# Optimization experiments

Hardware: AMD Instinct MI355X
Metric: run time of the kernel (lower is better)

## Reference

```python
import jax, jax.numpy as jnp
import numpy as np

N = 50000
E = 800000
D_IN = 128
D_OUT = 128


def setup_inputs() -> dict:
    key = jax.random.key(0)
    ks = jax.random.split(key, 12)
    x = jax.random.normal(ks[0], (N, D_IN), dtype=jnp.float32)
    W1 = jax.random.normal(ks[1], (D_IN, D_OUT), dtype=jnp.float32) * (1.0 / np.sqrt(D_IN))
    b1 = jnp.zeros((D_OUT,), dtype=jnp.float32)
    W2 = jax.random.normal(ks[2], (D_IN, D_OUT), dtype=jnp.float32) * (1.0 / np.sqrt(D_IN))
    b2 = jnp.zeros((D_OUT,), dtype=jnp.float32)
    # inverted-dropout masks, p=0.5 -> values in {0, 2}
    def mask(k):
        return jnp.where(jax.random.uniform(k, (N, D_IN)) < 0.5, 0.0, 2.0).astype(jnp.float32)
    mask_pos1 = mask(ks[3])
    mask_neg1 = mask(ks[4])
    mask_pos2 = mask(ks[5])
    mask_neg2 = mask(ks[6])
    edge_index1 = jax.random.randint(ks[7], (2, E), 0, N, dtype=jnp.int32)
    edge_index2 = jax.random.randint(ks[8], (2, E), 0, N, dtype=jnp.int32)
    perm1 = jax.random.permutation(ks[9], N).astype(jnp.int32)
    perm2 = jax.random.permutation(ks[10], N).astype(jnp.int32)
    return dict(x=x, W1=W1, b1=b1, W2=W2, b2=b2,
                mask_pos1=mask_pos1, mask_neg1=mask_neg1,
                mask_pos2=mask_pos2, mask_neg2=mask_neg2,
                edge_index1=edge_index1, edge_index2=edge_index2,
                perm1=perm1, perm2=perm2)


def gcn_conv(x, W, b, edge_index):
    """PyG GCNConv: add self-loops, symmetric normalization, then x@W aggregation + bias."""
    n = x.shape[0]
    xw = x @ W  # [N, D_OUT]
    loops = jnp.arange(n, dtype=edge_index.dtype)
    src = jnp.concatenate([edge_index[0], loops])
    dst = jnp.concatenate([edge_index[1], loops])
    deg = jax.ops.segment_sum(jnp.ones_like(dst, dtype=xw.dtype), dst, num_segments=n)
    dinv = jax.lax.rsqrt(jnp.maximum(deg, 1.0))  # deg >= 1 due to self-loops
    norm = dinv[src] * dinv[dst]                 # [E+N]
    msg = xw[src] * norm[:, None]                # [E+N, D_OUT]
    out = jax.ops.segment_sum(msg, dst, num_segments=n)
    return out + b


def _branch(x, W, b, edge_index, mask_pos, mask_neg, perm):
    pos_h = jax.nn.relu(gcn_conv(x * mask_pos, W, b, edge_index))
    neg_in = (x * mask_neg)[perm]
    neg_h = jax.nn.relu(gcn_conv(neg_in, W, b, edge_index))
    summary = jnp.mean(pos_h, axis=0, keepdims=True)  # [1, D_OUT]
    return pos_h, neg_h, summary


def reference(x, W1, b1, W2, b2, mask_pos1, mask_neg1, mask_pos2, mask_neg2,
              edge_index1, edge_index2, perm1, perm2):
    p1, n1, s1 = _branch(x, W1, b1, edge_index1, mask_pos1, mask_neg1, perm1)
    p2, n2, s2 = _branch(x, W2, b2, edge_index2, mask_pos2, mask_neg2, perm2)
    return (p1, n1, s1, p2, n2, s2)
```

## Files before the change

kernel.cpp:

```cpp
#include <hip/hip_runtime.h>
#include <hip/hip_fp16.h>

#define NN 50000
#define NE 800000
#define D 128
#define BKT_BLOCKS 1024
#define GEMM_BLOCKS 3128
#define NBKT 64
#define BW 782
#define SCAP 2048

typedef _Float16 half8_t __attribute__((ext_vector_type(8)));
typedef _Float16 half4_t __attribute__((ext_vector_type(4)));
typedef float f32x4 __attribute__((ext_vector_type(4)));

__global__ void k_init(float* s1, float* s2, int* bcnt,
                       const float* __restrict__ W1, const float* __restrict__ W2,
                       _Float16* wt1, _Float16* wt2,
                       const int* __restrict__ perm1, const int* __restrict__ perm2,
                       int* pinv1, int* pinv2) {
    int i = blockIdx.x * 256 + threadIdx.x;
    if (i < NN) { pinv1[perm1[i]] = i; pinv2[perm2[i]] = i; }
    if (i < 1024) bcnt[i] = 0;
    if (i < D) { s1[i] = 0.f; s2[i] = 0.f; }
    if (i < 16384) {
        int n = i >> 7, k = i & 127;
        wt1[n * 128 + k] = (_Float16)W1[k * 128 + n];
        wt2[n * 128 + k] = (_Float16)W2[k * 128 + n];
    }
}

__launch_bounds__(256)
__global__ void k_bucket_gemm(const int* __restrict__ src1, const int* __restrict__ dst1,
                              const int* __restrict__ src2, const int* __restrict__ dst2,
                              int* bcnt, int2* bsd1, int2* bsd2,
                              const _Float16* __restrict__ wt1, const _Float16* __restrict__ wt2,
                              const float* __restrict__ x,
                              const float* __restrict__ mp1, const float* __restrict__ mn1,
                              const float* __restrict__ mp2, const float* __restrict__ mn2,
                              const int* __restrict__ pinv1, const int* __restrict__ pinv2,
                              _Float16* xwi1, _Float16* xwi2) {
    __shared__ int lcnt[128], lpos[128], gbase[128];
    __shared__ __align__(16) _Float16 ST[4][16][136];
    int t = threadIdx.x;
    int bid = blockIdx.x;

    if (bid < BKT_BLOCKS) {
        int sl = bid & 7;
        if (t < 128) { lcnt[t] = 0; lpos[t] = 0; }
        __syncthreads();

        int e0 = bid * 256 + t;
        int s1v0=0,d1v0=0,s2v0=0,d2v0=0, s1v1=0,d1v1=0,s2v1=0,d2v1=0;
        int s1v2=0,d1v2=0,s2v2=0,d2v2=0, s1v3=0,d1v3=0,s2v3=0,d2v3=0;
        bool v0 = (e0 + 0 * 262144) < NE;
        bool v1 = (e0 + 1 * 262144) < NE;
        bool v2 = (e0 + 2 * 262144) < NE;
        bool v3 = (e0 + 3 * 262144) < NE;
        if (v0) { int e = e0;             s1v0 = src1[e]; d1v0 = dst1[e]; s2v0 = src2[e]; d2v0 = dst2[e]; }
        if (v1) { int e = e0 + 262144;    s1v1 = src1[e]; d1v1 = dst1[e]; s2v1 = src2[e]; d2v1 = dst2[e]; }
        if (v2) { int e = e0 + 2*262144;  s1v2 = src1[e]; d1v2 = dst1[e]; s2v2 = src2[e]; d2v2 = dst2[e]; }
        if (v3) { int e = e0 + 3*262144;  s1v3 = src1[e]; d1v3 = dst1[e]; s2v3 = src2[e]; d2v3 = dst2[e]; }

        if (v0) { atomicAdd(&lcnt[d1v0 / BW], 1); atomicAdd(&lcnt[NBKT + d2v0 / BW], 1); }
        if (v1) { atomicAdd(&lcnt[d1v1 / BW], 1); atomicAdd(&lcnt[NBKT + d2v1 / BW], 1); }
        if (v2) { atomicAdd(&lcnt[d1v2 / BW], 1); atomicAdd(&lcnt[NBKT + d2v2 / BW], 1); }
        if (v3) { atomicAdd(&lcnt[d1v3 / BW], 1); atomicAdd(&lcnt[NBKT + d2v3 / BW], 1); }
        __syncthreads();
        if (t < 128) gbase[t] = atomicAdd(&bcnt[t * 8 + sl], lcnt[t]);
        __syncthreads();

        #define PLACE(sv, dv) { \
            int r = (dv) / BW; \
            int p = gbase[r] + atomicAdd(&lpos[r], 1); \
            if (p < SCAP) bsd1[(r * 8 + sl) * SCAP + p] = make_int2((sv), (dv)); }
        #define PLACE2(sv, dv) { \
            int r = (dv) / BW; \
            int p = gbase[NBKT + r] + atomicAdd(&lpos[NBKT + r], 1); \
            if (p < SCAP) bsd2[(r * 8 + sl) * SCAP + p] = make_int2((sv), (dv)); }
        if (v0) { PLACE(s1v0, d1v0); PLACE2(s2v0, d2v0); }
        if (v1) { PLACE(s1v1, d1v1); PLACE2(s2v1, d2v1); }
        if (v2) { PLACE(s1v2, d1v2); PLACE2(s2v2, d2v2); }
        if (v3) { PLACE(s1v3, d1v3); PLACE2(s2v3, d2v3); }
        #undef PLACE
        #undef PLACE2
        return;
    }

    int g = bid - BKT_BLOCKS;
    int which = g / 782;
    int bx = g - which * 782;
    const _Float16* wt = (which < 2) ? wt1 : wt2;
    const float* mask = (which == 0) ? mp1 : (which == 1) ? mn1 : (which == 2) ? mp2 : mn2;
    const int* pinv = (which == 1) ? pinv1 : (which == 3) ? pinv2 : nullptr;
    _Float16* out = ((which < 2) ? xwi1 : xwi2) + ((which & 1) ? 128 : 0);

    int wave = t >> 6;
    int lane = t & 63;
    int quad = lane >> 4;
    int m = lane & 15;
    int tile = bx * 4 + wave;
    if (tile * 16 >= NN) return;

    int row = tile * 16 + m;
    const float* xrow = x + (long)row * D;
    const float* mrow = mask + (long)row * D;

    half8_t a[4];
    #pragma unroll
    for (int kk = 0; kk < 4; kk++) {
        int k0 = kk * 32 + quad * 8;
        f32x4 xa = *(const f32x4*)(xrow + k0);
        f32x4 xb = *(const f32x4*)(xrow + k0 + 4);
        f32x4 ma = __builtin_nontemporal_load((const f32x4*)(mrow + k0));
        f32x4 mb = __builtin_nontemporal_load((const f32x4*)(mrow + k0 + 4));
        a[kk][0] = (_Float16)(xa[0] * ma[0]);
        a[kk][1] = (_Float16)(xa[1] * ma[1]);
        a[kk][2] = (_Float16)(xa[2] * ma[2]);
        a[kk][3] = (_Float16)(xa[3] * ma[3]);
        a[kk][4] = (_Float16)(xb[0] * mb[0]);
        a[kk][5] = (_Float16)(xb[1] * mb[1]);
        a[kk][6] = (_Float16)(xb[2] * mb[2]);
        a[kk][7] = (_Float16)(xb[3] * mb[3]);
    }

    f32x4 accs[8];
    #pragma unroll
    for (int nt = 0; nt < 8; nt++) {
        const _Float16* wrow = wt + (nt * 16 + m) * 128 + quad * 8;
        f32x4 acc = {0.f, 0.f, 0.f, 0.f};
        #pragma unroll
        for (int kk = 0; kk < 4; kk++) {
            half8_t w = *(const half8_t*)(wrow + kk * 32);
            acc = __builtin_amdgcn_mfma_f32_16x16x32_f16(w, a[kk], acc, 0, 0, 0);
        }
        accs[nt] = acc;
    }

    int orow = pinv ? pinv[row] : row;
    _Float16* st = &ST[wave][0][0];

    #pragma unroll
    for (int nt = 0; nt < 8; nt++) {
        half4_t h;
        h[0] = (_Float16)accs[nt][0];
        h[1] = (_Float16)accs[nt][1];
        h[2] = (_Float16)accs[nt][2];
        h[3] = (_Float16)accs[nt][3];
        *(half4_t*)(st + m * 136 + nt * 16 + quad * 4) = h;
    }
    #pragma unroll
    for (int p = 0; p < 4; p++) {
        int cc = (lane >> 4) + p * 4;
        half8_t v = *(const half8_t*)(st + m * 136 + cc * 8);
        *(half8_t*)(out + (long)orow * 256 + cc * 8) = v;
    }
}

__launch_bounds__(512)
__global__ void k_build(const int* __restrict__ bcnt,
                        const int2* __restrict__ bsd1, const int2* __restrict__ bsd2,
                        int* rp1, int* rp2, int* col1, int* col2,
                        float* dinv1, float* dinv2) {
    __shared__ int h[1024];
    __shared__ int tsum[512];
    __shared__ int tb[64];
    __shared__ int ns[8];
    __shared__ int bbase;
    int t = threadIdx.x;
    int g = blockIdx.x >> 6;
    int f = blockIdx.x & 63;
    const int2* bsd = (g ? bsd2 : bsd1) + f * 8 * SCAP;
    int* rp = g ? rp2 : rp1;
    int* col = g ? col2 : col1;
    float* dinv = g ? dinv2 : dinv1;

    h[t] = 0; h[t + 512] = 0;
    if (t < 8) {
        int v = bcnt[(g * NBKT + f) * 8 + t];
        ns[t] = (v > SCAP) ? SCAP : v;
    }
    if (t < NBKT) {
        int tot = 0;
        #pragma unroll
        for (int s = 0; s < 8; s++) tot += bcnt[(g * NBKT + t) * 8 + s];
        tb[t] = tot;
    }
    __syncthreads();

    #pragma unroll
    for (int s = 0; s < 8; s++) {
        int n = ns[s];
        const int2* seg = bsd + s * SCAP;
        for (int i = t; i < n; i += 512) atomicAdd(&h[seg[i].y - f * BW], 1);
    }
    __syncthreads();
    if (t == 0) { int b = 0; for (int j = 0; j < f; j++) b += tb[j]; bbase = b; }

    int a0 = h[2 * t], a1 = h[2 * t + 1];
    int s = a0 + a1;
    tsum[t] = s;
    __syncthreads();
    for (int off = 1; off < 512; off <<= 1) {
        int add = (t >= off) ? tsum[t - off] : 0;
        __syncthreads();
        tsum[t] += add;
        __syncthreads();
    }
    int excl = tsum[t] - s + bbase;
    int idx = 2 * t, gd = f * BW + idx;
    int e0 = excl, e1 = excl + a0;
    h[2 * t] = e0; h[2 * t + 1] = e1;
    if (idx < BW && gd < NN)         { rp[gd]     = e0; dinv[gd]     = rsqrtf((float)(a0 + 1)); }
    if (idx + 1 < BW && gd + 1 < NN) { rp[gd + 1] = e1; dinv[gd + 1] = rsqrtf((float)(a1 + 1)); }
    if (f == 63 && t == 0) rp[NN] = NE;
    __syncthreads();

    #pragma unroll
    for (int sg = 0; sg < 8; sg++) {
        int n = ns[sg];
        const int2* seg = bsd + sg * SCAP;
        for (int i = t; i < n; i += 512) {
            int2 e = seg[i];
            int p = atomicAdd(&h[e.y - f * BW], 1);
            col[p] = e.x;
        }
    }
}

__launch_bounds__(256)
__global__ void k_agg(const _Float16* __restrict__ xwi1, const _Float16* __restrict__ xwi2,
                      const int* __restrict__ rp1, const int* __restrict__ col1,
                      const float* __restrict__ dinv1,
                      const int* __restrict__ rp2, const int* __restrict__ col2,
                      const float* __restrict__ dinv2,
                      const float* __restrict__ b1, const float* __restrict__ b2,
                      float* out) {
    int g = blockIdx.y;
    const _Float16* xwi = g ? xwi2 : xwi1;
    const int* rp = g ? rp2 : rp1;
    const int* col = g ? col2 : col1;
    const float* dinv = g ? dinv2 : dinv1;
    const float* bias = g ? b2 : b1;
    float* pos_out = out + (g ? 12800128L : 0L);
    float* neg_out = out + (g ? 19200128L : 6400000L);

    int t = threadIdx.x;
    int wave = t >> 6, lane = t & 63;
    int i = blockIdx.x * 4 + wave;
    if (i >= NN) return;
    int j4 = lane * 4;

    float di = dinv[i];
    half4_t sv = *(const half4_t*)(xwi + (long)i * 256 + j4);
    float a0 = di * (float)sv[0], a1 = di * (float)sv[1];
    float a2 = di * (float)sv[2], a3 = di * (float)sv[3];
    int e0 = rp[i], e1 = rp[i + 1];
    int e = e0;
    for (; e + 8 <= e1; e += 8) {
        int s0 = col[e + 0], s1 = col[e + 1], s2 = col[e + 2], s3 = col[e + 3];
        int s4 = col[e + 4], s5 = col[e + 5], s6 = col[e + 6], s7 = col[e + 7];
        float ds0 = dinv[s0], ds1 = dinv[s1], ds2 = dinv[s2], ds3 = dinv[s3];
        float ds4 = dinv[s4], ds5 = dinv[s5], ds6 = dinv[s6], ds7 = dinv[s7];
        half4_t v0 = *(const half4_t*)(xwi + (long)s0 * 256 + j4);
        half4_t v1 = *(const half4_t*)(xwi + (long)s1 * 256 + j4);
        half4_t v2 = *(const half4_t*)(xwi + (long)s2 * 256 + j4);
        half4_t v3 = *(const half4_t*)(xwi + (long)s3 * 256 + j4);
        half4_t v4 = *(const half4_t*)(xwi + (long)s4 * 256 + j4);
        half4_t v5 = *(const half4_t*)(xwi + (long)s5 * 256 + j4);
        half4_t v6 = *(const half4_t*)(xwi + (long)s6 * 256 + j4);
        half4_t v7 = *(const half4_t*)(xwi + (long)s7 * 256 + j4);
        a0 += ds0*(float)v0[0] + ds1*(float)v1[0] + ds2*(float)v2[0] + ds3*(float)v3[0]
            + ds4*(float)v4[0] + ds5*(float)v5[0] + ds6*(float)v6[0] + ds7*(float)v7[0];
        a1 += ds0*(float)v0[1] + ds1*(float)v1[1] + ds2*(float)v2[1] + ds3*(float)v3[1]
            + ds4*(float)v4[1] + ds5*(float)v5[1] + ds6*(float)v6[1] + ds7*(float)v7[1];
        a2 += ds0*(float)v0[2] + ds1*(float)v1[2] + ds2*(float)v2[2] + ds3*(float)v3[2]
            + ds4*(float)v4[2] + ds5*(float)v5[2] + ds6*(float)v6[2] + ds7*(float)v7[2];
        a3 += ds0*(float)v0[3] + ds1*(float)v1[3] + ds2*(float)v2[3] + ds3*(float)v3[3]
            + ds4*(float)v4[3] + ds5*(float)v5[3] + ds6*(float)v6[3] + ds7*(float)v7[3];
    }
    for (; e + 4 <= e1; e += 4) {
        int s0 = col[e + 0], s1 = col[e + 1], s2 = col[e + 2], s3 = col[e + 3];
        float ds0 = dinv[s0], ds1 = dinv[s1], ds2 = dinv[s2], ds3 = dinv[s3];
        half4_t v0 = *(const half4_t*)(xwi + (long)s0 * 256 + j4);
        half4_t v1 = *(const half4_t*)(xwi + (long)s1 * 256 + j4);
        half4_t v2 = *(const half4_t*)(xwi + (long)s2 * 256 + j4);
        half4_t v3 = *(const half4_t*)(xwi + (long)s3 * 256 + j4);
        a0 += ds0*(float)v0[0] + ds1*(float)v1[0] + ds2*(float)v2[0] + ds3*(float)v3[0];
        a1 += ds0*(float)v0[1] + ds1*(float)v1[1] + ds2*(float)v2[1] + ds3*(float)v3[1];
        a2 += ds0*(float)v0[2] + ds1*(float)v1[2] + ds2*(float)v2[2] + ds3*(float)v3[2];
        a3 += ds0*(float)v0[3] + ds1*(float)v1[3] + ds2*(float)v2[3] + ds3*(float)v3[3];
    }
    for (; e < e1; e++) {
        int s = col[e];
        float ds = dinv[s];
        half4_t v = *(const half4_t*)(xwi + (long)s * 256 + j4);
        a0 += ds*(float)v[0]; a1 += ds*(float)v[1]; a2 += ds*(float)v[2]; a3 += ds*(float)v[3];
    }
    int jj = (lane < 32) ? j4 : (j4 - 128);
    const f32x4* bp = (const f32x4*)(bias + jj);
    f32x4 bv = *bp;
    f32x4 o;
    o[0] = fmaxf(0.f, di * a0 + bv[0]);
    o[1] = fmaxf(0.f, di * a1 + bv[1]);
    o[2] = fmaxf(0.f, di * a2 + bv[2]);
    o[3] = fmaxf(0.f, di * a3 + bv[3]);
    float* dst = ((lane < 32) ? pos_out : neg_out) + (long)i * D + jj;
    __builtin_nontemporal_store(o, (f32x4*)dst);
}

__launch_bounds__(256)
__global__ void k_sum(const float* __restrict__ pos1, const float* __restrict__ pos2,
                      float* s1, float* s2) {
    int g = blockIdx.y;
    const float* pos = g ? pos2 : pos1;
    float* s = g ? s2 : s1;
    int t = threadIdx.x;
    int rg = t >> 5;
    int j = (t & 31) * 4;
    f32x4 acc = {0.f, 0.f, 0.f, 0.f};
    for (int i = blockIdx.x * 8 + rg; i < NN; i += gridDim.x * 8) {
        f32x4 v = __builtin_nontemporal_load((const f32x4*)(pos + (long)i * D + j));
        acc[0] += v[0]; acc[1] += v[1]; acc[2] += v[2]; acc[3] += v[3];
    }
    __shared__ float sm[8][128];
    sm[rg][j + 0] = acc[0];
    sm[rg][j + 1] = acc[1];
    sm[rg][j + 2] = acc[2];
    sm[rg][j + 3] = acc[3];
    __syncthreads();
    if (t < 128) {
        float v = 0.f;
        for (int r = 0; r < 8; r++) v += sm[r][t];
        atomicAdd(&s[t], v * (1.0f / NN));
    }
}

extern "C" void kernel_launch(void* const* d_in, const int* in_sizes, int n_in,
                              void* d_out, int out_size, void* d_ws, size_t ws_size,
                              hipStream_t stream) {
    const float* x   = (const float*)d_in[0];
    const float* W1  = (const float*)d_in[1];
    const float* b1  = (const float*)d_in[2];
    const float* W2  = (const float*)d_in[3];
    const float* b2  = (const float*)d_in[4];
    const float* mp1 = (const float*)d_in[5];
    const float* mn1 = (const float*)d_in[6];
    const float* mp2 = (const float*)d_in[7];
    const float* mn2 = (const float*)d_in[8];
    const int* e1 = (const int*)d_in[9];
    const int* e2 = (const int*)d_in[10];
    const int* perm1 = (const int*)d_in[11];
    const int* perm2 = (const int*)d_in[12];
    const int* src1 = e1;       const int* dst1 = e1 + NE;
    const int* src2 = e2;       const int* dst2 = e2 + NE;
    float* out = (float*)d_out;

    char* w = (char*)d_ws;
    _Float16* xwi1 = (_Float16*)w; w += (size_t)NN * 256 * 2;
    _Float16* xwi2 = (_Float16*)w; w += (size_t)NN * 256 * 2;
    int* rp1 = (int*)w;   w += (size_t)(NN + 4) * 4;
    int* rp2 = (int*)w;   w += (size_t)(NN + 4) * 4;
    int* col1 = (int*)w;  w += (size_t)NE * 4;
    int* col2 = (int*)w;  w += (size_t)NE * 4;
    float* dinv1 = (float*)w; w += (size_t)NN * 4;
    float* dinv2 = (float*)w; w += (size_t)NN * 4;
    int* bcnt  = (int*)w; w += (size_t)1024 * 4;
    int2* bsd1 = (int2*)w; w += (size_t)NBKT * 8 * SCAP * 8;
    int2* bsd2 = (int2*)w; w += (size_t)NBKT * 8 * SCAP * 8;
    _Float16* wt1 = (_Float16*)w; w += (size_t)D * D * 2;
    _Float16* wt2 = (_Float16*)w; w += (size_t)D * D * 2;
    int* pinv1 = (int*)w; w += (size_t)NN * 4;
    int* pinv2 = (int*)w; w += (size_t)NN * 4;

    float* s1 = out + 12800000L;
    float* s2 = out + 25600128L;
    const float* pos1 = out;
    const float* pos2 = out + 12800128L;

    k_init<<<dim3(196), 256, 0, stream>>>(s1, s2, bcnt, W1, W2, wt1, wt2,
                                          perm1, perm2, pinv1, pinv2);
    k_bucket_gemm<<<dim3(BKT_BLOCKS + GEMM_BLOCKS), 256, 0, stream>>>(
        src1, dst1, src2, dst2, bcnt, bsd1, bsd2,
        wt1, wt2, x, mp1, mn1, mp2, mn2, pinv1, pinv2, xwi1, xwi2);
    k_build<<<dim3(128), 512, 0, stream>>>(bcnt, bsd1, bsd2,
                                           rp1, rp2, col1, col2, dinv1, dinv2);
    k_agg<<<dim3(12500, 2), 256, 0, stream>>>(xwi1, xwi2,
                                              rp1, col1, dinv1, rp2, col2, dinv2,
                                              b1, b2, out);
    k_sum<<<dim3(512, 2), 256, 0, stream>>>(pos1, pos2, s1, s2);
}
```

Before: 454.7 us.

## Sub-bucket edges by source octant instead of block slice for gather locality

Edges were previously split into 64 destination buckets, each with 8 sub-slices chosen by block id. They are now binned by destination bucket and also by source-node octant (src/6250), giving 512 bins per graph. Edges in each sub-bucket therefore share a narrow source range, which should improve cache locality when the aggregation gathers source rows. In exchange, the bucketing needs 1024-entry shared counters (unioned with the GEMM staging tile), more global atomics per block, and has a higher risk of a bin overflowing SCAP.

```diff
diff --git a/kernel.cpp b/kernel.cpp
--- a/kernel.cpp
+++ b/kernel.cpp
@@ -8,6 +8,7 @@
 #define GEMM_BLOCKS 3128
 #define NBKT 64
 #define BW 782
+#define OCT 6250
 #define SCAP 2048
 
 typedef _Float16 half8_t __attribute__((ext_vector_type(8)));
@@ -40,14 +41,16 @@
                               const float* __restrict__ mp2, const float* __restrict__ mn2,
                               const int* __restrict__ pinv1, const int* __restrict__ pinv2,
                               _Float16* xwi1, _Float16* xwi2) {
-    __shared__ int lcnt[128], lpos[128], gbase[128];
-    __shared__ __align__(16) _Float16 ST[4][16][136];
+    __shared__ __align__(16) union SU {
+        struct { int lcnt[1024], lpos[1024], gbase[1024]; } b;
+        _Float16 st[4][16][136];
+    } U;
     int t = threadIdx.x;
     int bid = blockIdx.x;
 
     if (bid < BKT_BLOCKS) {
-        int sl = bid & 7;
-        if (t < 128) { lcnt[t] = 0; lpos[t] = 0; }
+        #pragma unroll
+        for (int q = 0; q < 4; q++) { U.b.lcnt[t + q * 256] = 0; U.b.lpos[t + q * 256] = 0; }
         __syncthreads();
 
         int e0 = bid * 256 + t;
@@ -62,28 +65,37 @@
         if (v2) { int e = e0 + 2*262144;  s1v2 = src1[e]; d1v2 = dst1[e]; s2v2 = src2[e]; d2v2 = dst2[e]; }
         if (v3) { int e = e0 + 3*262144;  s1v3 = src1[e]; d1v3 = dst1[e]; s2v3 = src2[e]; d2v3 = dst2[e]; }
 
-        if (v0) { atomicAdd(&lcnt[d1v0 / BW], 1); atomicAdd(&lcnt[NBKT + d2v0 / BW], 1); }
-        if (v1) { atomicAdd(&lcnt[d1v1 / BW], 1); atomicAdd(&lcnt[NBKT + d2v1 / BW], 1); }
-        if (v2) { atomicAdd(&lcnt[d1v2 / BW], 1); atomicAdd(&lcnt[NBKT + d2v2 / BW], 1); }
-        if (v3) { atomicAdd(&lcnt[d1v3 / BW], 1); atomicAdd(&lcnt[NBKT + d2v3 / BW], 1); }
+        #define BIN1(sv, dv) (((dv) / BW) * 8 + (sv) / OCT)
+        #define BIN2(sv, dv) (512 + ((dv) / BW) * 8 + (sv) / OCT)
+        if (v0) { atomicAdd(&U.b.lcnt[BIN1(s1v0, d1v0)], 1); atomicAdd(&U.b.lcnt[BIN2(s2v0, d2v0)], 1); }
+        if (v1) { atomicAdd(&U.b.lcnt[BIN1(s1v1, d1v1)], 1); atomicAdd(&U.b.lcnt[BIN2(s2v1, d2v1)], 1); }
+        if (v2) { atomicAdd(&U.b.lcnt[BIN1(s1v2, d1v2)], 1); atomicAdd(&U.b.lcnt[BIN2(s2v2, d2v2)], 1); }
+        if (v3) { atomicAdd(&U.b.lcnt[BIN1(s1v3, d1v3)], 1); atomicAdd(&U.b.lcnt[BIN2(s2v3, d2v3)], 1); }
         __syncthreads();
-        if (t < 128) gbase[t] = atomicAdd(&bcnt[t * 8 + sl], lcnt[t]);
+        #pragma unroll
+        for (int q = 0; q < 4; q++) {
+            int idx = t + q * 256;
+            int c = U.b.lcnt[idx];
+            U.b.gbase[idx] = c ? atomicAdd(&bcnt[idx], c) : 0;
+        }
         __syncthreads();
 
         #define PLACE(sv, dv) { \
-            int r = (dv) / BW; \
-            int p = gbase[r] + atomicAdd(&lpos[r], 1); \
-            if (p < SCAP) bsd1[(r * 8 + sl) * SCAP + p] = make_int2((sv), (dv)); }
+            int bin = BIN1(sv, dv); \
+            int p = U.b.gbase[bin] + atomicAdd(&U.b.lpos[bin], 1); \
+            if (p < SCAP) bsd1[bin * SCAP + p] = make_int2((sv), (dv)); }
         #define PLACE2(sv, dv) { \
-            int r = (dv) / BW; \
-            int p = gbase[NBKT + r] + atomicAdd(&lpos[NBKT + r], 1); \
-            if (p < SCAP) bsd2[(r * 8 + sl) * SCAP + p] = make_int2((sv), (dv)); }
+            int bin = BIN2(sv, dv); \
+            int p = U.b.gbase[bin] + atomicAdd(&U.b.lpos[bin], 1); \
+            if (p < SCAP) bsd2[(bin - 512) * SCAP + p] = make_int2((sv), (dv)); }
         if (v0) { PLACE(s1v0, d1v0); PLACE2(s2v0, d2v0); }
         if (v1) { PLACE(s1v1, d1v1); PLACE2(s2v1, d2v1); }
         if (v2) { PLACE(s1v2, d1v2); PLACE2(s2v2, d2v2); }
         if (v3) { PLACE(s1v3, d1v3); PLACE2(s2v3, d2v3); }
         #undef PLACE
         #undef PLACE2
+        #undef BIN1
+        #undef BIN2
         return;
     }
 
@@ -138,7 +150,7 @@
     }
 
     int orow = pinv ? pinv[row] : row;
-    _Float16* st = &ST[wave][0][0];
+    _Float16* st = &U.st[wave][0][0];
 
     #pragma unroll
     for (int nt = 0; nt < 8; nt++) {
```

Result: slower. 486.2 us (+6.9%).
